# Kernel tuning notes

Measured on AMD Instinct MI355X. Metric: run time of the kernel, lower is better.

The kernel has to match this reference:

```python
import jax, jax.numpy as jnp
import numpy as np

ATTN_SPLITS = 2
TEMPERATURE = 10000.0

# ---------- split / merge helpers (faithful to split_feature / merge_splits) ----------

def split_cf(x, ns):  # channel-first [b,c,h,w] -> [b*ns*ns, c, h/ns, w/ns]
    b, c, h, w = x.shape
    x = x.reshape(b, c, ns, h // ns, ns, w // ns).transpose(0, 2, 4, 1, 3, 5)
    return x.reshape(b * ns * ns, c, h // ns, w // ns)

def merge_cf(x, ns):  # channel-first inverse
    b, c, h, w = x.shape
    nb = b // (ns * ns)
    x = x.reshape(nb, ns, ns, c, h, w).transpose(0, 3, 1, 4, 2, 5)
    return x.reshape(nb, c, ns * h, ns * w)

def split_cl(x, ns):  # channel-last [b,h,w,c] -> [b*ns*ns, h/ns, w/ns, c]
    b, h, w, c = x.shape
    x = x.reshape(b, ns, h // ns, ns, w // ns, c).transpose(0, 1, 3, 2, 4, 5)
    return x.reshape(b * ns * ns, h // ns, w // ns, c)

def merge_cl(x, ns):  # channel-last inverse
    b, h, w, c = x.shape
    nb = b // (ns * ns)
    x = x.reshape(nb, ns, ns, h, w, c).transpose(0, 1, 3, 2, 4, 5)
    return x.reshape(nb, ns * h, ns * w, c)

# ---------- PositionEmbeddingSine (normalize=True, scale=2*pi) ----------

def pos_embed_sine(h, w, num_pos_feats):
    scale = 2.0 * np.pi
    eps = 1e-6
    ones = jnp.ones((h, w), jnp.float32)
    y_embed = jnp.cumsum(ones, 0)
    x_embed = jnp.cumsum(ones, 1)
    y_embed = y_embed / (y_embed[-1:, :] + eps) * scale
    x_embed = x_embed / (x_embed[:, -1:] + eps) * scale
    dim_t = jnp.arange(num_pos_feats, dtype=jnp.float32)
    dim_t = TEMPERATURE ** (2.0 * jnp.floor(dim_t / 2.0) / num_pos_feats)
    pos_x = x_embed[:, :, None] / dim_t  # [h,w,npf]
    pos_y = y_embed[:, :, None] / dim_t
    pos_x = jnp.stack([jnp.sin(pos_x[:, :, 0::2]), jnp.cos(pos_x[:, :, 1::2])], -1).reshape(h, w, -1)
    pos_y = jnp.stack([jnp.sin(pos_y[:, :, 0::2]), jnp.cos(pos_y[:, :, 1::2])], -1).reshape(h, w, -1)
    pos = jnp.concatenate([pos_y, pos_x], -1)  # [h,w,c]
    return jnp.transpose(pos, (2, 0, 1))[None]  # [1,c,h,w]

def feature_add_position(f0, f1, attn_splits, c):
    if attn_splits > 1:
        f0s = split_cf(f0, attn_splits)
        f1s = split_cf(f1, attn_splits)
        pos = pos_embed_sine(f0s.shape[2], f0s.shape[3], c // 2)
        return merge_cf(f0s + pos, attn_splits), merge_cf(f1s + pos, attn_splits)
    pos = pos_embed_sine(f0.shape[2], f0.shape[3], c // 2)
    return f0 + pos, f1 + pos

# ---------- shifted-window attention mask (static, numpy) ----------

def shift_window_attn_mask(h, w, ns):
    wsh, wsw = h // ns, w // ns
    ssh, ssw = wsh // 2, wsw // 2
    img = np.zeros((h, w), np.float32)
    cnt = 0
    for hs in (slice(0, -wsh), slice(-wsh, -ssh), slice(-ssh, None)):
        for ws in (slice(0, -wsw), slice(-wsw, -ssw), slice(-ssw, None)):
            img[hs, ws] = cnt
            cnt += 1
    m = img.reshape(ns, wsh, ns, wsw).transpose(0, 2, 1, 3).reshape(ns * ns, wsh * wsw)
    am = m[:, None, :] - m[:, :, None]
    am = np.where(am != 0, -100.0, 0.0).astype(np.float32)
    return jnp.asarray(am)  # [ns*ns, N, N]

# ---------- single-head split (shifted) window attention ----------

def split_window_attention(q, k, v, ns, h, w, attn_mask):
    b, _, c = q.shape
    bn = b * ns * ns
    wsh, wsw = h // ns, w // ns
    ssh, ssw = wsh // 2, wsw // 2
    q = q.reshape(b, h, w, c)
    k = k.reshape(b, h, w, c)
    v = v.reshape(b, h, w, c)
    q = jnp.roll(q, (-ssh, -ssw), (1, 2))
    k = jnp.roll(k, (-ssh, -ssw), (1, 2))
    v = jnp.roll(v, (-ssh, -ssw), (1, 2))
    qs = split_cl(q, ns).reshape(bn, -1, c)
    ks = split_cl(k, ns).reshape(bn, -1, c)
    vs = split_cl(v, ns).reshape(bn, -1, c)
    scores = jnp.einsum('bnc,bmc->bnm', qs, ks) / jnp.sqrt(jnp.asarray(c, qs.dtype))
    scores = scores + jnp.tile(attn_mask, (b, 1, 1))
    attn = jax.nn.softmax(scores, axis=-1)
    out = jnp.einsum('bnm,bmc->bnc', attn, vs)
    out = merge_cl(out.reshape(bn, wsh, wsw, c), ns)
    out = jnp.roll(out, (ssh, ssw), (1, 2))
    return out.reshape(b, -1, c)

# ---------- global correlation softmax matching ----------

def global_correlation_softmax(f0, f1):
    b, c, h, w = f0.shape
    f0v = f0.reshape(b, c, -1)  # [b,c,hw]
    f1v = f1.reshape(b, c, -1)
    corr = jnp.einsum('bcn,bcm->bnm', f0v, f1v) / jnp.sqrt(jnp.asarray(c, f0.dtype))
    yy, xx = jnp.meshgrid(jnp.arange(h), jnp.arange(w), indexing='ij')
    grid = jnp.stack([xx, yy], 0).astype(f0.dtype)  # [2,h,w] (x,y)
    gridv = grid.reshape(2, -1).T  # [hw,2]
    prob = jax.nn.softmax(corr, axis=-1)
    corresp = jnp.einsum('bnm,md->bnd', prob, gridv).reshape(b, h, w, 2).transpose(0, 3, 1, 2)
    flow = corresp - grid[None]
    return flow

# ---------- setup & reference ----------

def setup_inputs() -> dict:
    key = jax.random.key(0)
    k0, k1 = jax.random.split(key)
    b, c, h, w = 4, 128, 64, 64
    feature0 = jax.random.normal(k0, (b, c, h, w), jnp.float32)
    feature1 = jax.random.normal(k1, (b, c, h, w), jnp.float32)
    return {'feature0': feature0, 'feature1': feature1}

def reference(feature0, feature1):
    b, c, h, w = feature0.shape
    ns = ATTN_SPLITS
    f0, f1 = feature_add_position(feature0, feature1, ns, c)
    attn_mask = shift_window_attn_mask(h, w, ns)
    q = f0.reshape(b, c, -1).transpose(0, 2, 1)  # [b,hw,c]
    kv = f1.reshape(b, c, -1).transpose(0, 2, 1)
    f0_attn = split_window_attention(q, kv, kv, ns, h, w, attn_mask)  # [b,hw,c]
    f0_attn = f0_attn.transpose(0, 2, 1).reshape(b, c, h, w)
    flow = global_correlation_softmax(f0_attn, f1)  # [b,2,h,w]
    return flow
```

## Files before the change

### kernel.cpp

```cpp
#include <hip/hip_runtime.h>
#include <hip/hip_bf16.h>
#include <math.h>

#define NB 4
#define NC 128
#define NH 64
#define NW 64
#define NHW 4096
#define SCALE 0.08838834764831845f
#define PSL2E 0.12753102543365835f

typedef short bf16x8 __attribute__((ext_vector_type(8)));
typedef float f32x4 __attribute__((ext_vector_type(4)));

__device__ __forceinline__ unsigned bfbits(float f) {
    unsigned u = __float_as_uint(f);
    return (u + 0x7FFFu + ((u >> 16) & 1u)) >> 16;
}
__device__ __forceinline__ unsigned bfpair(float a, float b) {
    return bfbits(a) | (bfbits(b) << 16);
}

__global__ __launch_bounds__(256) void pos_kernel(float* __restrict__ pos) {
    int idx = blockIdx.x * 256 + threadIdx.x;
    if (idx >= NC * 32 * 32) return;
    int x = idx & 31;
    int y = (idx >> 5) & 31;
    int c = idx >> 10;
    const float twopi = 6.283185307179586f;
    const float denom = 32.0f + 1e-6f;
    int cc = (c < 64) ? c : (c - 64);
    float e = (c < 64) ? (float)(y + 1) : (float)(x + 1);
    e = e * (twopi / denom);
    int k = cc >> 1;
    float arg = e * exp2f(-0.41524101186091903f * (float)k);
    pos[idx] = (cc & 1) ? cosf(arg) : sinf(arg);
}

__global__ __launch_bounds__(256) void pack_kernel(
        const float* __restrict__ f0, const float* __restrict__ f1,
        const float* __restrict__ pos,
        __hip_bfloat16* __restrict__ F0t, __hip_bfloat16* __restrict__ Bt,
        __hip_bfloat16* __restrict__ Ktw) {
    __shared__ float T[64][129];
    int blk = blockIdx.x;
    const bool isA = blk < 256;
    const float* src = isA ? f0 : f1;
    blk &= 255;
    const int y = blk & 63;
    const int b = blk >> 6;
    const int tid = threadIdx.x;
    const float* s = src + (size_t)b * NC * NHW + y * 64;
    const float sA = isA ? PSL2E : 1.0f;
    for (int idx = tid; idx < 64 * NC; idx += 256) {
        const int x = idx & 63, c = idx >> 6;
        T[x][c] = (s[c * NHW + x] + pos[(c << 10) + ((y & 31) << 5) + (x & 31)]) * sA;
    }
    __syncthreads();
    __hip_bfloat16* dst = isA ? F0t : Bt;
    for (int idx = tid; idx < 512; idx += 256) {
        const int x = idx >> 3, c0 = (idx & 7) * 16;
        const float* tr = &T[x][c0];
        uint4 v0, v1;
        v0.x = bfpair(tr[0], tr[1]);   v0.y = bfpair(tr[2], tr[3]);
        v0.z = bfpair(tr[4], tr[5]);   v0.w = bfpair(tr[6], tr[7]);
        v1.x = bfpair(tr[8], tr[9]);   v1.y = bfpair(tr[10], tr[11]);
        v1.z = bfpair(tr[12], tr[13]); v1.w = bfpair(tr[14], tr[15]);
        __hip_bfloat16* row = dst + ((size_t)b * NHW + y * 64 + x) * NC + c0;
        *reinterpret_cast<uint4*>(row) = v0;
        *reinterpret_cast<uint4*>(row + 8) = v1;
    }
    if (!isA) {
        const int yp = (y + 48) & 63;
        const int wi = yp >> 5, ry = yp & 31;
        const int c = tid >> 1;
        const int wj = tid & 1;
        const int win = b * 4 + wi * 2 + wj;
        unsigned up[16];
        #pragma unroll
        for (int pr = 0; pr < 16; ++pr) {
            const int x0 = ((wj << 5) + 2 * pr + 16) & 63;
            up[pr] = bfpair(T[x0][c], T[x0 + 1][c]);
        }
        __hip_bfloat16* krow = Ktw + ((size_t)win * NC + c) * 1024 + ry * 32;
        uint4* uv = reinterpret_cast<uint4*>(up);
        #pragma unroll
        for (int i = 0; i < 4; ++i)
            *reinterpret_cast<uint4*>(krow + i * 8) = uv[i];
    }
}

__global__ __launch_bounds__(256) void attn_mfma_kernel(
        const __hip_bfloat16* __restrict__ F0t,
        const __hip_bfloat16* __restrict__ Bt,
        const __hip_bfloat16* __restrict__ Ktw,
        __hip_bfloat16* __restrict__ At) {
    __shared__ __align__(16) char lds[73728];
    char* KsB = lds;
    char* VsB = lds + 32768;
    char* Pscr = lds + 65536;
    const int tid = threadIdx.x;
    const int lane = tid & 63;
    const int w = tid >> 6;
    const int l15 = lane & 15;
    const int g = lane >> 4;
    const int blk = blockIdx.x;
    const int win = blk >> 4;
    const int qt = blk & 15;
    const int b = win >> 2, wi = (win >> 1) & 1, wj = win & 1;

    const char* Btb = (const char*)(Bt + (size_t)b * NHW * NC);
    const char* Vsrc = (const char*)(Ktw + (size_t)win * NC * 1024);

    bf16x8 qf[4];
    {
        const int tok = qt * 64 + w * 16 + l15;
        const int yo = ((wi << 5) + (tok >> 5) + 16) & 63;
        const int xo = ((wj << 5) + (tok & 31) + 16) & 63;
        const __hip_bfloat16* qrow =
            F0t + ((size_t)b * NHW + yo * 64 + xo) * NC + g * 8;
        #pragma unroll
        for (int kk = 0; kk < 4; ++kk)
            qf[kk] = *reinterpret_cast<const bf16x8*>(qrow + kk * 32);
    }

    const int reg_q = (wi ? (qt < 8 ? 1 : 2) : 0) * 3
                    + (wj ? ((w & 1) == 0 ? 1 : 2) : 0);

    auto stageK = [&](int buf, int kt) {
        char* dst = KsB + buf * 16384;
        #pragma unroll
        for (int it = 0; it < 4; ++it) {
            const int obase = w * 4096 + it * 1024;
            const int row = w * 16 + it * 4 + (lane >> 4);
            const int tok = kt * 64 + row;
            const int yo = ((wi << 5) + (tok >> 5) + 16) & 63;
            const int xo = ((wj << 5) + (tok & 31) + 16) & 63;
            const char* src = Btb + (yo * 64 + xo) * 256 +
                              (((lane & 15) * 16) ^ ((row & 7) << 4));
            __builtin_amdgcn_global_load_lds(
                (const __attribute__((address_space(1))) void*)src,
                (__attribute__((address_space(3))) void*)(dst + obase), 16, 0, 0);
        }
    };
    auto stageV = [&](int buf, int kt) {
        char* dst = VsB + buf * 16384;
        #pragma unroll
        for (int it = 0; it < 4; ++it) {
            const int obase = w * 4096 + it * 1024;
            const int o = obase + lane * 16;
            const int crow = o >> 7;
            const int off = o & 127;
            __builtin_amdgcn_global_load_lds(
                (const __attribute__((address_space(1))) void*)(Vsrc + crow * 2048 + kt * 128 + (off ^ ((crow & 7) << 4))),
                (__attribute__((address_space(3))) void*)(dst + obase), 16, 0, 0);
        }
    };

    f32x4 oacc[8] = {{0,0,0,0},{0,0,0,0},{0,0,0,0},{0,0,0,0},
                     {0,0,0,0},{0,0,0,0},{0,0,0,0},{0,0,0,0}};
    float zacc = 0.f;

    stageK(0, 0); stageV(0, 0);
    __syncthreads();

    for (int kt = 0; kt < 16; ++kt) {
        const int buf = kt & 1;
        if (kt < 15) { stageK(buf ^ 1, kt + 1); stageV(buf ^ 1, kt + 1); }

        const char* kb = KsB + buf * 16384;
        f32x4 sacc[4] = {{0,0,0,0},{0,0,0,0},{0,0,0,0},{0,0,0,0}};
        #pragma unroll
        for (int kk = 0; kk < 4; ++kk) {
            #pragma unroll
            for (int msub = 0; msub < 4; ++msub) {
                const int byte = msub * 4096 + l15 * 256 + ((kk * 64 + g * 16) ^ ((l15 & 7) << 4));
                bf16x8 kf = *reinterpret_cast<const bf16x8*>(kb + byte);
                sacc[msub] = __builtin_amdgcn_mfma_f32_16x16x32_bf16(kf, qf[kk], sacc[msub], 0, 0, 0);
            }
        }

        const int rk_row = (wi ? (kt < 8 ? 1 : 2) : 0) * 3;
        char* pw = Pscr + w * 2048;
        #pragma unroll
        for (int msub = 0; msub < 4; ++msub) {
            const int rk = rk_row + (wj ? ((msub & 1) == 0 ? 1 : 2) : 0);
            const bool ok = (rk == reg_q);
            const float p0 = ok ? exp2f(sacc[msub][0]) : 0.f;
            const float p1 = ok ? exp2f(sacc[msub][1]) : 0.f;
            const float p2 = ok ? exp2f(sacc[msub][2]) : 0.f;
            const float p3 = ok ? exp2f(sacc[msub][3]) : 0.f;
            zacc += (p0 + p1) + (p2 + p3);
            *reinterpret_cast<unsigned*>(pw + l15 * 128 + ((msub * 32 + g * 8 + 0) ^ ((l15 & 7) << 4))) = bfpair(p0, p1);
            *reinterpret_cast<unsigned*>(pw + l15 * 128 + ((msub * 32 + g * 8 + 4) ^ ((l15 & 7) << 4))) = bfpair(p2, p3);
        }
        bf16x8 pf[2];
        #pragma unroll
        for (int kk = 0; kk < 2; ++kk)
            pf[kk] = *reinterpret_cast<const bf16x8*>(pw + l15 * 128 + ((kk * 64 + g * 16) ^ ((l15 & 7) << 4)));

        const char* vb = VsB + buf * 16384;
        #pragma unroll
        for (int kk = 0; kk < 2; ++kk) {
            #pragma unroll
            for (int co = 0; co < 8; ++co) {
                const int byte = (co * 16 + l15) * 128 + ((kk * 64 + g * 16) ^ ((l15 & 7) << 4));
                bf16x8 vf = *reinterpret_cast<const bf16x8*>(vb + byte);
                oacc[co] = __builtin_amdgcn_mfma_f32_16x16x32_bf16(pf[kk], vf, oacc[co], 0, 0, 0);
            }
        }
        __syncthreads();
    }

    float z = zacc;
    z += __shfl_xor(z, 16);
    z += __shfl_xor(z, 32);

    unsigned short* olds = reinterpret_cast<unsigned short*>(lds + w * 4096);
    #pragma unroll
    for (int r = 0; r < 4; ++r) {
        const float zi = PSL2E / __shfl(z, g * 4 + r);
        #pragma unroll
        for (int co = 0; co < 8; ++co)
            olds[(g * 4 + r) * 128 + co * 16 + l15] = (unsigned short)bfbits(oacc[co][r] * zi);
    }

    const int qloc = lane >> 2;
    const int c0 = (lane & 3) * 32;
    const int tok = qt * 64 + w * 16 + qloc;
    const int yo = ((wi << 5) + (tok >> 5) + 16) & 63;
    const int xo = ((wj << 5) + (tok & 31) + 16) & 63;
    __hip_bfloat16* arow = At + ((size_t)b * NHW + yo * 64 + xo) * NC + c0;
    #pragma unroll
    for (int i = 0; i < 4; ++i) {
        int4 v = *reinterpret_cast<const int4*>(olds + qloc * 128 + c0 + i * 8);
        *reinterpret_cast<int4*>(arow + i * 8) = v;
    }
}

__global__ __launch_bounds__(256) void corr_part_kernel(
        const __hip_bfloat16* __restrict__ At,
        const __hip_bfloat16* __restrict__ Bt,
        float4* __restrict__ part) {
    __shared__ __hip_bfloat16 Bs[2][64 * 128];
    const int tid = threadIdx.x;
    const int lane = tid & 63;
    const int w = tid >> 6;
    const int blk = blockIdx.x;
    const int ms = blk & 15;
    const int nt = (blk >> 4) & 31;
    const int b = blk >> 9;
    const int l15 = lane & 15;
    const int g = lane >> 4;
    const int n0 = nt * 128 + w * 32;

    const __hip_bfloat16* Ab = At + (size_t)b * NHW * NC;
    const __hip_bfloat16* Bb = Bt + (size_t)b * NHW * NC;

    bf16x8 afrag[2][4];
    #pragma unroll
    for (int s = 0; s < 2; ++s) {
        const __hip_bfloat16* arow = Ab + (size_t)(n0 + s * 16 + l15) * NC + g * 8;
        #pragma unroll
        for (int kk = 0; kk < 4; ++kk)
            afrag[s][kk] = *reinterpret_cast<const bf16x8*>(arow + kk * 32);
    }

    auto stage = [&](int buf, int mtile) {
        const char* srcbase = reinterpret_cast<const char*>(Bb + (size_t)mtile * 64 * NC);
        #pragma unroll
        for (int it = 0; it < 4; ++it) {
            const int obase = w * 4096 + it * 1024;
            const int o = obase + lane * 16;
            const int row = o >> 8;
            const int off = o & 255;
            const char* src = srcbase + row * 256 + (off ^ ((row & 7) << 4));
            __builtin_amdgcn_global_load_lds(
                (const __attribute__((address_space(1))) void*)src,
                (__attribute__((address_space(3))) void*)((char*)&Bs[buf][0] + obase),
                16, 0, 0);
        }
    };

    f32x4 rl[2]  = {{0,0,0,0},{0,0,0,0}};
    f32x4 rsm[2] = {{0,0,0,0},{0,0,0,0}};
    f32x4 rsy[2] = {{0,0,0,0},{0,0,0,0}};

    stage(0, ms * 4);
    __syncthreads();

    for (int mt = 0; mt < 4; ++mt) {
        const int buf = mt & 1;
        if (mt < 3) stage(buf ^ 1, ms * 4 + mt + 1);

        f32x4 acc[2][4] = {{{0,0,0,0},{0,0,0,0},{0,0,0,0},{0,0,0,0}},
                           {{0,0,0,0},{0,0,0,0},{0,0,0,0},{0,0,0,0}}};
        const char* base = (const char*)&Bs[buf][0];
        #pragma unroll
        for (int kk = 0; kk < 4; ++kk) {
            #pragma unroll
            for (int msub = 0; msub < 4; ++msub) {
                const int byte = msub * 4096 + l15 * 256 +
                                 ((kk * 64 + g * 16) ^ ((l15 & 7) << 4));
                bf16x8 bfrag = *reinterpret_cast<const bf16x8*>(base + byte);
                acc[0][msub] = __builtin_amdgcn_mfma_f32_16x16x32_bf16(
                    afrag[0][kk], bfrag, acc[0][msub], 0, 0, 0);
                acc[1][msub] = __builtin_amdgcn_mfma_f32_16x16x32_bf16(
                    afrag[1][kk], bfrag, acc[1][msub], 0, 0, 0);
            }
        }
        const float y0 = (float)(ms * 4 + mt);
        #pragma unroll
        for (int s = 0; s < 2; ++s) {
            #pragma unroll
            for (int r = 0; r < 4; ++r) {
                float p0 = exp2f(acc[s][0][r]);
                float p1 = exp2f(acc[s][1][r]);
                float p2 = exp2f(acc[s][2][r]);
                float p3 = exp2f(acc[s][3][r]);
                float ts = (p0 + p1) + (p2 + p3);
                rl[s][r]  += ts;
                rsy[s][r] += y0 * ts;
                rsm[s][r] += fmaf(3.f, p3, fmaf(2.f, p2, p1));
            }
        }
        __syncthreads();
    }

    const float xl = (float)l15;
    #pragma unroll
    for (int s = 0; s < 2; ++s) {
        #pragma unroll
        for (int r = 0; r < 4; ++r) {
            float a  = rl[s][r];
            float sx = xl * rl[s][r] + 16.f * rsm[s][r];
            float sy = rsy[s][r];
            #pragma unroll
            for (int m = 1; m < 16; m <<= 1) {
                a  += __shfl_xor(a, m);
                sx += __shfl_xor(sx, m);
                sy += __shfl_xor(sy, m);
            }
            if (l15 == 0) {
                const int n = n0 + s * 16 + g * 4 + r;
                part[((size_t)b * NHW + n) * 16 + ms] = make_float4(a, sx, sy, 0.f);
            }
        }
    }
}

__global__ __launch_bounds__(256) void finalize_kernel(
        const float4* __restrict__ part, float* __restrict__ out) {
    const int idx = blockIdx.x * 256 + threadIdx.x;
    if (idx >= NB * NHW) return;
    const int n = idx & (NHW - 1);
    const int b = idx >> 12;
    float l = 0.f, sx = 0.f, sy = 0.f;
    #pragma unroll
    for (int i = 0; i < 16; ++i) {
        float4 p = part[(size_t)idx * 16 + i];
        l += p.x; sx += p.y; sy += p.z;
    }
    const float inv = 1.0f / l;
    out[(size_t)b * 2 * NHW + n]       = sx * inv - (float)(n & 63);
    out[(size_t)b * 2 * NHW + NHW + n] = sy * inv - (float)(n >> 6);
}

extern "C" void kernel_launch(void* const* d_in, const int* in_sizes, int n_in,
                              void* d_out, int out_size, void* d_ws, size_t ws_size,
                              hipStream_t stream) {
    const float* f0 = (const float*)d_in[0];
    const float* f1 = (const float*)d_in[1];
    float* pos = (float*)d_ws;
    __hip_bfloat16* F0t = (__hip_bfloat16*)(pos + 131072);
    __hip_bfloat16* Bt  = F0t + (size_t)NB * NHW * NC;
    __hip_bfloat16* Ktw = Bt  + (size_t)NB * NHW * NC;
    __hip_bfloat16* At  = Ktw + (size_t)16 * NC * 1024;
    float4* part = (float4*)(At + (size_t)NB * NHW * NC);
    float* out = (float*)d_out;

    pos_kernel<<<512, 256, 0, stream>>>(pos);
    pack_kernel<<<512, 256, 0, stream>>>(f0, f1, pos, F0t, Bt, Ktw);
    attn_mfma_kernel<<<256, 256, 0, stream>>>(F0t, Bt, Ktw, At);
    corr_part_kernel<<<2048, 256, 0, stream>>>(At, Bt, part);
    finalize_kernel<<<64, 256, 0, stream>>>(part, out);
}
```

Baseline: 82.38 us.

## Give each wave a private double-buffered B pipeline in correlation kernel

Rewrites the correlation kernel so each wave streams its own 16-row B tiles into a private LDS slice with double buffering. It uses vmcnt waits instead of block-wide barriers and covers twice as many key columns per block, which halves the grid and the number of partial sums finalize must reduce. The aim is to remove __syncthreads stalls and cut partial-output traffic. In exchange, every wave reloads the same B data, so L2 traffic per block rises, and the per-tile MFMA work gets smaller.

```diff
diff --git a/kernel.cpp b/kernel.cpp
--- a/kernel.cpp
+++ b/kernel.cpp
@@ -242,20 +242,21 @@
         const __hip_bfloat16* __restrict__ At,
         const __hip_bfloat16* __restrict__ Bt,
         float4* __restrict__ part) {
-    __shared__ __hip_bfloat16 Bs[2][64 * 128];
+    __shared__ __align__(16) char S[32768];
     const int tid = threadIdx.x;
     const int lane = tid & 63;
     const int w = tid >> 6;
     const int blk = blockIdx.x;
-    const int ms = blk & 15;
-    const int nt = (blk >> 4) & 31;
-    const int b = blk >> 9;
+    const int ms = blk & 7;
+    const int nt = (blk >> 3) & 31;
+    const int b = blk >> 8;
     const int l15 = lane & 15;
     const int g = lane >> 4;
     const int n0 = nt * 128 + w * 32;
 
     const __hip_bfloat16* Ab = At + (size_t)b * NHW * NC;
-    const __hip_bfloat16* Bb = Bt + (size_t)b * NHW * NC;
+    const char* Bb = (const char*)(Bt + (size_t)b * NHW * NC);
+    char* myLDS = S + w * 8192;
 
     bf16x8 afrag[2][4];
     #pragma unroll
@@ -266,84 +267,81 @@
             afrag[s][kk] = *reinterpret_cast<const bf16x8*>(arow + kk * 32);
     }
 
-    auto stage = [&](int buf, int mtile) {
-        const char* srcbase = reinterpret_cast<const char*>(Bb + (size_t)mtile * 64 * NC);
+    auto stage = [&](int buf, int t) {
+        const char* srcbase = Bb + (size_t)(ms * 512 + t * 16) * 256;
+        char* dst = myLDS + buf * 4096;
         #pragma unroll
         for (int it = 0; it < 4; ++it) {
-            const int obase = w * 4096 + it * 1024;
-            const int o = obase + lane * 16;
+            const int o = it * 1024 + lane * 16;
             const int row = o >> 8;
             const int off = o & 255;
-            const char* src = srcbase + row * 256 + (off ^ ((row & 7) << 4));
             __builtin_amdgcn_global_load_lds(
-                (const __attribute__((address_space(1))) void*)src,
-                (__attribute__((address_space(3))) void*)((char*)&Bs[buf][0] + obase),
-                16, 0, 0);
+                (const __attribute__((address_space(1))) void*)(srcbase + row * 256 + (off ^ ((row & 7) << 4))),
+                (__attribute__((address_space(3))) void*)(dst + it * 1024), 16, 0, 0);
         }
     };
 
     f32x4 rl[2]  = {{0,0,0,0},{0,0,0,0}};
-    f32x4 rsm[2] = {{0,0,0,0},{0,0,0,0}};
+    f32x4 rsx[2] = {{0,0,0,0},{0,0,0,0}};
     f32x4 rsy[2] = {{0,0,0,0},{0,0,0,0}};
-
-    stage(0, ms * 4);
-    __syncthreads();
-
-    for (int mt = 0; mt < 4; ++mt) {
-        const int buf = mt & 1;
-        if (mt < 3) stage(buf ^ 1, ms * 4 + mt + 1);
-
-        f32x4 acc[2][4] = {{{0,0,0,0},{0,0,0,0},{0,0,0,0},{0,0,0,0}},
-                           {{0,0,0,0},{0,0,0,0},{0,0,0,0},{0,0,0,0}}};
-        const char* base = (const char*)&Bs[buf][0];
+    const int mb0 = ms * 512;
+
+    auto compute = [&](int buf, int t) {
+        const char* base = myLDS + buf * 4096;
+        bf16x8 bfrag[4];
+        #pragma unroll
+        for (int kk = 0; kk < 4; ++kk)
+            bfrag[kk] = *reinterpret_cast<const bf16x8*>(
+                base + l15 * 256 + ((kk * 64 + g * 16) ^ ((l15 & 7) << 4)));
+        f32x4 acc[2] = {{0,0,0,0},{0,0,0,0}};
         #pragma unroll
         for (int kk = 0; kk < 4; ++kk) {
-            #pragma unroll
-            for (int msub = 0; msub < 4; ++msub) {
-                const int byte = msub * 4096 + l15 * 256 +
-                                 ((kk * 64 + g * 16) ^ ((l15 & 7) << 4));
-                bf16x8 bfrag = *reinterpret_cast<const bf16x8*>(base + byte);
-                acc[0][msub] = __builtin_amdgcn_mfma_f32_16x16x32_bf16(
-                    afrag[0][kk], bfrag, acc[0][msub], 0, 0, 0);
-                acc[1][msub] = __builtin_amdgcn_mfma_f32_16x16x32_bf16(
-                    afrag[1][kk], bfrag, acc[1][msub], 0, 0, 0);
-            }
-        }
-        const float y0 = (float)(ms * 4 + mt);
+            acc[0] = __builtin_amdgcn_mfma_f32_16x16x32_bf16(afrag[0][kk], bfrag[kk], acc[0], 0, 0, 0);
+            acc[1] = __builtin_amdgcn_mfma_f32_16x16x32_bf16(afrag[1][kk], bfrag[kk], acc[1], 0, 0, 0);
+        }
+        const int m = mb0 + t * 16;
+        const float cx = (float)((m & 63) + l15);
+        const float cy = (float)(m >> 6);
         #pragma unroll
         for (int s = 0; s < 2; ++s) {
             #pragma unroll
             for (int r = 0; r < 4; ++r) {
-                float p0 = exp2f(acc[s][0][r]);
-                float p1 = exp2f(acc[s][1][r]);
-                float p2 = exp2f(acc[s][2][r]);
-                float p3 = exp2f(acc[s][3][r]);
-                float ts = (p0 + p1) + (p2 + p3);
-                rl[s][r]  += ts;
-                rsy[s][r] += y0 * ts;
-                rsm[s][r] += fmaf(3.f, p3, fmaf(2.f, p2, p1));
-            }
-        }
-        __syncthreads();
-    }
-
-    const float xl = (float)l15;
+                const float p = exp2f(acc[s][r]);
+                rl[s][r]  += p;
+                rsx[s][r] = fmaf(cx, p, rsx[s][r]);
+                rsy[s][r] = fmaf(cy, p, rsy[s][r]);
+            }
+        }
+    };
+
+    stage(0, 0);
+    for (int t = 0; t < 31; ++t) {
+        const int buf = t & 1;
+        stage(buf ^ 1, t + 1);
+        asm volatile("s_waitcnt vmcnt(4)" ::: "memory");
+        __builtin_amdgcn_sched_barrier(0);
+        compute(buf, t);
+    }
+    asm volatile("s_waitcnt vmcnt(0)" ::: "memory");
+    __builtin_amdgcn_sched_barrier(0);
+    compute(31 & 1, 31);
+
     #pragma unroll
     for (int s = 0; s < 2; ++s) {
         #pragma unroll
         for (int r = 0; r < 4; ++r) {
             float a  = rl[s][r];
-            float sx = xl * rl[s][r] + 16.f * rsm[s][r];
+            float sx = rsx[s][r];
             float sy = rsy[s][r];
             #pragma unroll
-            for (int m = 1; m < 16; m <<= 1) {
-                a  += __shfl_xor(a, m);
-                sx += __shfl_xor(sx, m);
-                sy += __shfl_xor(sy, m);
+            for (int m2 = 1; m2 < 16; m2 <<= 1) {
+                a  += __shfl_xor(a, m2);
+                sx += __shfl_xor(sx, m2);
+                sy += __shfl_xor(sy, m2);
             }
             if (l15 == 0) {
                 const int n = n0 + s * 16 + g * 4 + r;
-                part[((size_t)b * NHW + n) * 16 + ms] = make_float4(a, sx, sy, 0.f);
+                part[((size_t)b * NHW + n) * 8 + ms] = make_float4(a, sx, sy, 0.f);
             }
         }
     }
@@ -357,8 +355,8 @@
     const int b = idx >> 12;
     float l = 0.f, sx = 0.f, sy = 0.f;
     #pragma unroll
-    for (int i = 0; i < 16; ++i) {
-        float4 p = part[(size_t)idx * 16 + i];
+    for (int i = 0; i < 8; ++i) {
+        float4 p = part[(size_t)idx * 8 + i];
         l += p.x; sx += p.y; sy += p.z;
     }
     const float inv = 1.0f / l;
@@ -382,6 +380,6 @@
     pos_kernel<<<512, 256, 0, stream>>>(pos);
     pack_kernel<<<512, 256, 0, stream>>>(f0, f1, pos, F0t, Bt, Ktw);
     attn_mfma_kernel<<<256, 256, 0, stream>>>(F0t, Bt, Ktw, At);
-    corr_part_kernel<<<2048, 256, 0, stream>>>(At, Bt, part);
+    corr_part_kernel<<<1024, 256, 0, stream>>>(At, Bt, part);
     finalize_kernel<<<64, 256, 0, stream>>>(part, out);
 }
```

New measurement: 79.59 us. 3.4% less time.
